# Performance work log

Hardware: AMD Instinct MI355X
Metric: run time of the kernel (lower is better)

The kernel has to match this reference:

```python
import jax, jax.numpy as jnp
import numpy as np

N = 40000          # nodes
E = 640000         # edges (avg in-degree ~16)
D_IN = 128         # in_dim == out_dim
E_DIM = 16         # edge feature dim
N_AGG = 6          # mean max min std dir1-av dir1-dx
N_SC = 3           # identity amplification attenuation
AVG_D_LOG = float(np.log(16.0))  # avg_d['log']
EPS = 1e-8
STD_EPS = 1e-5


def setup_inputs() -> dict:
    key = jax.random.key(0)
    ks = jax.random.split(key, 10)
    h = jax.random.normal(ks[0], (N, D_IN), jnp.float32)
    e = jax.random.normal(ks[1], (E, E_DIM), jnp.float32)
    eig = jax.random.normal(ks[2], (N, 2), jnp.float32)
    snorm_n = jax.random.uniform(ks[3], (N, 1), jnp.float32)
    src = jax.random.randint(ks[4], (E,), 0, N)
    dst = jax.random.randint(ks[5], (E,), 0, N)
    pre_in = 2 * D_IN + E_DIM
    W_pre = jax.random.normal(ks[6], (pre_in, D_IN), jnp.float32) / np.sqrt(pre_in)
    b_pre = jnp.zeros((D_IN,), jnp.float32)
    post_in = (N_AGG * N_SC + 1) * D_IN
    W_post = jax.random.normal(ks[7], (post_in, D_IN), jnp.float32) / np.sqrt(post_in)
    b_post = jnp.zeros((D_IN,), jnp.float32)
    return {"h": h, "e": e, "eig": eig, "snorm_n": snorm_n, "src": src,
            "dst": dst, "W_pre": W_pre, "b_pre": b_pre,
            "W_post": W_post, "b_post": b_post}


def reference(h, e, eig, snorm_n, src, dst, W_pre, b_pre, W_post, b_post):
    # --- pretrans on edges: MLP(cat(h_src, h_dst, ef)) -> [E, D_IN]
    z = jnp.concatenate([h[src], h[dst], e], axis=1)
    m = z @ W_pre + b_pre

    seg = lambda x: jax.ops.segment_sum(x, dst, num_segments=N)
    deg = seg(jnp.ones((E,), m.dtype))          # in-degree per node [N]
    has = deg > 0
    degc = jnp.maximum(deg, 1.0)

    # --- mailbox aggregators (edge-parallel segment reductions over dst)
    s1 = seg(m)
    mean = s1 / degc[:, None]
    var = seg(m * m) / degc[:, None] - mean * mean
    std = jnp.sqrt(jnp.maximum(var, 0.0) + STD_EPS)
    mx = jnp.where(has[:, None], jax.ops.segment_max(m, dst, num_segments=N), 0.0)
    mn = jnp.where(has[:, None], jax.ops.segment_min(m, dst, num_segments=N), 0.0)
    # eigenvector-directional aggregators (eig index 1), normalized per dst
    d = eig[src, 1] - eig[dst, 1]                              # [E]
    denom = seg(jnp.abs(d)) + EPS                              # [N]
    dir_av = seg(m * (jnp.abs(d) / denom[dst])[:, None])
    dir_dx = seg(m * (d / denom[dst])[:, None]) - h            # uses h_in

    agg = jnp.concatenate([mean, mx, mn, std, dir_av, dir_dx], axis=1)
    agg = jnp.where(has[:, None], agg, 0.0)  # DGL leaves zeros for isolated nodes

    # --- degree scalers: identity / amplification / attenuation
    logd = jnp.log(degc + 1.0)
    amp = agg * (logd / AVG_D_LOG)[:, None]
    att = agg * (AVG_D_LOG / logd)[:, None]
    hcat = jnp.concatenate([h, agg, amp, att], axis=1)  # [N, 19*D_IN]

    # --- posttrans MLP + graph norm + relu + residual (dropout p=0, no batchnorm)
    out = hcat @ W_post + b_post
    out = out * snorm_n
    out = jax.nn.relu(out)
    out = h + out
    return out
```

## Files before the change

kernel.cpp:

```cpp
#include <hip/hip_runtime.h>
#include <hip/hip_bf16.h>
#include <math.h>

typedef __attribute__((ext_vector_type(4))) float f32x4;
typedef __attribute__((ext_vector_type(2))) float f32x2;
typedef __attribute__((ext_vector_type(8))) short short8;
typedef unsigned short ushort_t;
typedef unsigned int uint_t;

__device__ __forceinline__ float b2f(unsigned short u) {
    unsigned int v = ((unsigned int)u) << 16;
    return __uint_as_float(v);
}
__device__ __forceinline__ unsigned short f2b(float f) {
    unsigned int x = __float_as_uint(f);
    unsigned int r = (x + 0x7fffu + ((x >> 16) & 1u)) >> 16;
    return (unsigned short)r;
}

__global__ void prep_kernel(const float* __restrict__ W_pre,
                            const float* __restrict__ W_post,
                            const float* __restrict__ h,
                            int* __restrict__ counts,
                            ushort_t* __restrict__ WbT,
                            ushort_t* __restrict__ WcT,
                            ushort_t* __restrict__ X, int Nn) {
    int i = blockIdx.x * 256 + threadIdx.x;
    int n0 = Nn + 1;
    if (i < n0) { counts[i] = 0; return; }
    i -= n0;
    if (i < 256 * 128) {
        int nn = i >> 7, k = i & 127;
        float v = (nn < 128) ? W_pre[k * 128 + nn] : W_pre[(128 + k) * 128 + (nn - 128)];
        WbT[i] = f2b(v);
        return;
    }
    i -= 256 * 128;
    if (i < 384 * 896) {
        int nn = i / 896, k = i % 896;
        float v;
        if (k < 128) {
            v = (nn < 128) ? W_post[k * 128 + nn] : 0.f;
        } else {
            int ka = k - 128;
            if (nn < 128)      v = W_post[(128 + ka) * 128 + nn];
            else if (nn < 256) v = W_post[(896 + ka) * 128 + (nn - 128)];
            else               v = W_post[(1664 + ka) * 128 + (nn - 256)];
        }
        WcT[i] = f2b(v);
        return;
    }
    i -= 384 * 896;
    if (i < Nn * 32) {
        int n = i >> 5, c4 = (i & 31) * 4;
        float4 hv = *(const float4*)&h[(size_t)n * 128 + c4];
        ushort4 o;
        o.x = f2b(hv.x); o.y = f2b(hv.y); o.z = f2b(hv.z); o.w = f2b(hv.w);
        *(ushort4*)&X[(size_t)n * 896 + c4] = o;
    }
}

__global__ void hist_kernel(const int* __restrict__ dst, int* __restrict__ counts, int E) {
    int i = blockIdx.x * 256 + threadIdx.x;
    if (i < E) atomicAdd(&counts[dst[i]], 1);
}

__global__ __launch_bounds__(256) void scanA_kernel(const int* __restrict__ counts,
                                                    int* __restrict__ localscan,
                                                    int* __restrict__ blocksum, int Nn) {
    __shared__ int part[256];
    int b = blockIdx.x, t = threadIdx.x;
    int idx = b * 1024 + t * 4;
    int4 v = (idx + 3 < Nn) ? *(const int4*)&counts[idx]
             : make_int4(idx < Nn ? counts[idx] : 0,
                         idx + 1 < Nn ? counts[idx + 1] : 0,
                         idx + 2 < Nn ? counts[idx + 2] : 0,
                         idx + 3 < Nn ? counts[idx + 3] : 0);
    int s1 = v.x, s2 = v.x + v.y, s3 = s2 + v.z, tot = s3 + v.w;
    part[t] = tot;
    __syncthreads();
    for (int off = 1; off < 256; off <<= 1) {
        int x = part[t];
        int u = (t >= off) ? part[t - off] : 0;
        __syncthreads();
        part[t] = x + u;
        __syncthreads();
    }
    int pre = (t > 0) ? part[t - 1] : 0;
    if (idx < Nn) {
        if (idx + 3 < Nn) {
            *(int4*)&localscan[idx] = make_int4(pre, pre + s1, pre + s2, pre + s3);
        } else {
            localscan[idx] = pre;
            if (idx + 1 < Nn) localscan[idx + 1] = pre + s1;
            if (idx + 2 < Nn) localscan[idx + 2] = pre + s2;
        }
    }
    if (t == 255) blocksum[b] = part[255];
}

__global__ __launch_bounds__(64) void scanB_kernel(int* __restrict__ blocksum, int nb) {
    __shared__ int sh[64];
    int t = threadIdx.x;
    int v = (t < nb) ? blocksum[t] : 0;
    sh[t] = v;
    __syncthreads();
    for (int off = 1; off < 64; off <<= 1) {
        int x = sh[t];
        int u = (t >= off) ? sh[t - off] : 0;
        __syncthreads();
        sh[t] = x + u;
        __syncthreads();
    }
    int pre = (t > 0) ? sh[t - 1] : 0;
    if (t < nb) blocksum[t] = pre;
    if (t == 63) blocksum[nb] = sh[63];
}

__global__ void scanC_kernel(int* __restrict__ localscan, const int* __restrict__ blocksum,
                             int* __restrict__ counts, int Nn, int nb) {
    int i = blockIdx.x * 256 + threadIdx.x;
    if (i < Nn) {
        int o = localscan[i] + blocksum[blockIdx.x >> 2];
        counts[i] = o;
        localscan[i] = o;
    }
    if (i == 0) counts[Nn] = blocksum[nb];
}

__global__ void scatter_kernel(const int* __restrict__ dst, const int* __restrict__ src,
                               const float* __restrict__ eig, int* __restrict__ cursors,
                               int4* __restrict__ esl, int E) {
    int i = blockIdx.x * 256 + threadIdx.x;
    if (i < E) {
        int v = dst[i];
        int p = atomicAdd(&cursors[v], 1);
        int s = src[i];
        esl[p] = make_int4(s, i, __float_as_int(eig[s * 2 + 1]), 0);
    }
}

template <int OUT_BF16>
__global__ __launch_bounds__(256) void gemm_bt(const ushort_t* __restrict__ A, int lda,
                                               const ushort_t* __restrict__ Bt, int ldb,
                                               void* __restrict__ Cv, int ldc,
                                               int M, int K, int NT) {
    __shared__ ushort_t ldsbuf[2 * 128 * 64];
    const int tid = threadIdx.x, wid = tid >> 6, lane = tid & 63;
    int nwg = gridDim.x;
    int orig = blockIdx.x;
    int q8 = nwg >> 3, r8 = nwg & 7;
    int xcd = orig & 7, local = orig >> 3;
    int wg = (xcd < r8 ? xcd * (q8 + 1) : r8 * (q8 + 1) + (xcd - r8) * q8) + local;
    const int m0 = (wg / NT) * 128, n0 = (wg % NT) * 128;
    f32x4 acc[4][4] = {};
    const int wrow = (wid >> 1) * 64, wcol = (wid & 1) * 64;

    for (int kt = 0; kt < K; kt += 64) {
#pragma unroll
        for (int rnd = 0; rnd < 4; ++rnd) {
            int libase = rnd * 256 + wid * 64;
            {
                int lc = libase + lane;
                int r = lc >> 3, cs = lc & 7;
                int c = cs ^ (r & 7);
                int row = m0 + r; row = row < M ? row : M - 1;
                const ushort_t* g = A + (size_t)row * lda + (kt + c * 8);
                __builtin_amdgcn_global_load_lds(
                    (const __attribute__((address_space(1))) unsigned int*)g,
                    (__attribute__((address_space(3))) unsigned int*)&ldsbuf[(size_t)libase * 8],
                    16, 0, 0);
            }
            {
                int lc = libase + lane;
                int r = lc >> 3, cs = lc & 7;
                int c = cs ^ (r & 7);
                const ushort_t* g = Bt + (size_t)(n0 + r) * ldb + (kt + c * 8);
                __builtin_amdgcn_global_load_lds(
                    (const __attribute__((address_space(1))) unsigned int*)g,
                    (__attribute__((address_space(3))) unsigned int*)&ldsbuf[8192 + (size_t)libase * 8],
                    16, 0, 0);
            }
        }
        __syncthreads();
#pragma unroll
        for (int kk = 0; kk < 2; ++kk) {
            short8 af[4], bfr[4];
#pragma unroll
            for (int f = 0; f < 4; ++f) {
                int r = wrow + f * 16 + (lane & 15);
                int c16 = kk * 4 + (lane >> 4);
                int ch = r * 8 + (c16 ^ (r & 7));
                af[f] = *(const short8*)&ldsbuf[ch * 8];
            }
#pragma unroll
            for (int f = 0; f < 4; ++f) {
                int r = wcol + f * 16 + (lane & 15);
                int c16 = kk * 4 + (lane >> 4);
                int ch = r * 8 + (c16 ^ (r & 7));
                bfr[f] = *(const short8*)&ldsbuf[8192 + ch * 8];
            }
#pragma unroll
            for (int i = 0; i < 4; ++i)
#pragma unroll
                for (int j = 0; j < 4; ++j)
                    acc[i][j] = __builtin_amdgcn_mfma_f32_16x16x32_bf16(af[i], bfr[j], acc[i][j], 0, 0, 0);
        }
        __syncthreads();
    }
#pragma unroll
    for (int i = 0; i < 4; ++i)
#pragma unroll
        for (int j = 0; j < 4; ++j)
#pragma unroll
            for (int q = 0; q < 4; ++q) {
                int row = m0 + wrow + i * 16 + (lane >> 4) * 4 + q;
                int col = n0 + wcol + j * 16 + (lane & 15);
                if (row < M) {
                    if (OUT_BF16) ((ushort_t*)Cv)[(size_t)row * ldc + col] = f2b(acc[i][j][q]);
                    else          ((float*)Cv)[(size_t)row * ldc + col] = acc[i][j][q];
                }
            }
}

#define RLI(v, l) __builtin_amdgcn_readlane((v), (l))
__global__ __launch_bounds__(256) void agg_coop(
    const ushort_t* __restrict__ PQ, ushort_t* __restrict__ X,
    const int4* __restrict__ esl, const int* __restrict__ offs,
    const float* __restrict__ eig, const float* __restrict__ h,
    const float* __restrict__ ef, const float* __restrict__ W_pre,
    const float* __restrict__ b_pre, float* __restrict__ scal, int Nn) {
    int tid = threadIdx.x;
    int wid = tid >> 6, lane = tid & 63;
    int n = blockIdx.x * 4 + wid;
    if (n >= Nn) return;
    int off0 = offs[n], off1 = offs[n + 1];
    int deg = off1 - off0;
    int d0 = lane * 2;

    f32x2 w3r[16];
#pragma unroll
    for (int j = 0; j < 16; ++j)
        w3r[j] = *(const f32x2*)&W_pre[(256 + j) * 128 + d0];

    uint_t qw = *(const uint_t*)&PQ[(size_t)n * 256 + 128 + d0];
    float2 bp = *(const float2*)&b_pre[d0];
    f32x2 qb;
    qb.x = b2f((ushort_t)(qw & 0xffff)) + bp.x;
    qb.y = b2f((ushort_t)(qw >> 16)) + bp.y;
    float eigd = eig[n * 2 + 1];

    f32x2 s = {0.f, 0.f}, ss = {0.f, 0.f}, av = {0.f, 0.f}, dv = {0.f, 0.f};
    f32x2 mx = {-1e30f, -1e30f}, mn = {1e30f, 1e30f};
    float den = 0.f;

    for (int q0 = off0; q0 < off1; q0 += 16) {
        int cnt = off1 - q0; if (cnt > 16) cnt = 16;
        int slot = q0 + (lane & 15);
        if (slot > off1 - 1) slot = off1 - 1;
        int4 rc = esl[slot];
        int eidL = __shfl(rc.y, lane >> 2);
        float4 efv = ((const float4*)ef)[(size_t)eidL * 4 + (lane & 3)];
        uint_t pw[16];
#pragma unroll
        for (int j = 0; j < 16; ++j) {
            if (j < cnt) {
                int sj = RLI(rc.x, j);
                pw[j] = *(const uint_t*)&PQ[(size_t)sj * 256 + d0];
            }
        }
#pragma unroll
        for (int j = 0; j < 16; ++j) {
            if (j < cnt) {
                f32x2 acc = qb;
#pragma unroll
                for (int b = 0; b < 4; ++b) {
                    float va = __uint_as_float((uint_t)RLI(__float_as_int(efv.x), 4 * j + b));
                    float vb = __uint_as_float((uint_t)RLI(__float_as_int(efv.y), 4 * j + b));
                    float vc = __uint_as_float((uint_t)RLI(__float_as_int(efv.z), 4 * j + b));
                    float vd = __uint_as_float((uint_t)RLI(__float_as_int(efv.w), 4 * j + b));
                    acc = va * w3r[4 * b + 0] + acc;
                    acc = vb * w3r[4 * b + 1] + acc;
                    acc = vc * w3r[4 * b + 2] + acc;
                    acc = vd * w3r[4 * b + 3] + acc;
                }
                f32x2 m;
                m.x = b2f((ushort_t)(pw[j] & 0xffff));
                m.y = b2f((ushort_t)(pw[j] >> 16));
                m = m + acc;
                float dd = __int_as_float(RLI(rc.z, j)) - eigd;
                float ad = fabsf(dd);
                s = s + m; ss = m * m + ss;
                mx = __builtin_elementwise_max(mx, m);
                mn = __builtin_elementwise_min(mn, m);
                av = ad * m + av; dv = dd * m + dv;
                den += ad;
            }
        }
    }

    size_t xb = (size_t)n * 896 + 128;
    float2 hv = *(const float2*)&h[(size_t)n * 128 + d0];
    float o[12];
    if (deg > 0) {
        float inv = 1.f / (float)deg;
        float mean0 = s.x * inv, mean1 = s.y * inv;
        float var0 = fmaxf(ss.x * inv - mean0 * mean0, 0.f);
        float var1 = fmaxf(ss.y * inv - mean1 * mean1, 0.f);
        float sd0 = sqrtf(var0 + 1e-5f), sd1 = sqrtf(var1 + 1e-5f);
        float idn = 1.f / (den + 1e-8f);
        o[0] = mean0; o[1] = mean1; o[2] = mx.x; o[3] = mx.y; o[4] = mn.x; o[5] = mn.y;
        o[6] = sd0; o[7] = sd1; o[8] = av.x * idn; o[9] = av.y * idn;
        o[10] = dv.x * idn - hv.x; o[11] = dv.y * idn - hv.y;
    } else {
#pragma unroll
        for (int k = 0; k < 12; ++k) o[k] = 0.f;
    }
#pragma unroll
    for (int a = 0; a < 6; ++a) {
        uint_t w = (uint_t)f2b(o[2 * a]) | ((uint_t)f2b(o[2 * a + 1]) << 16);
        *(uint_t*)&X[xb + a * 128 + d0] = w;
    }
    if (lane == 0) {
        float degc = deg > 0 ? (float)deg : 1.f;
        float logd = logf(degc + 1.f);
        scal[n * 2] = logd * (1.f / 2.772588722239781f);
        scal[n * 2 + 1] = 2.772588722239781f / logd;
    }
}

__global__ __launch_bounds__(256) void epilogue_kernel(
    const ushort_t* __restrict__ O3, const float* __restrict__ h,
    const float* __restrict__ snorm, const float* __restrict__ scal,
    const float* __restrict__ b_post, float* __restrict__ out, int Nn) {
    int g = blockIdx.x * 256 + threadIdx.x;
    if (g >= Nn * 32) return;
    int n = g >> 5, c4 = (g & 31) * 4;
    float a = scal[n * 2], b = scal[n * 2 + 1], sn = snorm[n];
    const ushort_t* base = O3 + (size_t)n * 384 + c4;
    ushort4 u1 = *(const ushort4*)base;
    ushort4 u2 = *(const ushort4*)(base + 128);
    ushort4 u3 = *(const ushort4*)(base + 256);
    float4 bp = *(const float4*)&b_post[c4];
    float4 hv = *(const float4*)&h[(size_t)n * 128 + c4];
    float4 r;
    r.x = fmaxf((b2f(u1.x) + a * b2f(u2.x) + b * b2f(u3.x) + bp.x) * sn, 0.f) + hv.x;
    r.y = fmaxf((b2f(u1.y) + a * b2f(u2.y) + b * b2f(u3.y) + bp.y) * sn, 0.f) + hv.y;
    r.z = fmaxf((b2f(u1.z) + a * b2f(u2.z) + b * b2f(u3.z) + bp.z) * sn, 0.f) + hv.z;
    r.w = fmaxf((b2f(u1.w) + a * b2f(u2.w) + b * b2f(u3.w) + bp.w) * sn, 0.f) + hv.w;
    *(float4*)&out[(size_t)n * 128 + c4] = r;
}

extern "C" void kernel_launch(void* const* d_in, const int* in_sizes, int n_in,
                              void* d_out, int out_size, void* d_ws, size_t ws_size,
                              hipStream_t stream) {
    const float* h      = (const float*)d_in[0];
    const float* ef     = (const float*)d_in[1];
    const float* eig    = (const float*)d_in[2];
    const float* snorm  = (const float*)d_in[3];
    const int*   src    = (const int*)d_in[4];
    const int*   dst    = (const int*)d_in[5];
    const float* W_pre  = (const float*)d_in[6];
    const float* b_pre  = (const float*)d_in[7];
    const float* W_post = (const float*)d_in[8];
    const float* b_post = (const float*)d_in[9];
    int Nn = in_sizes[0] / 128;
    int E  = in_sizes[4];
    float* out = (float*)d_out;

    char* ws = (char*)d_ws;
    size_t off = 0;
    auto alloc = [&](size_t bytes) {
        size_t o = off;
        off = (off + bytes + 255) & ~(size_t)255;
        return o;
    };
    size_t o_counts  = alloc(((size_t)Nn + 1) * 4);
    size_t o_cursors = alloc((size_t)Nn * 4);
    size_t o_bsum    = alloc(65 * 4);
    size_t o_esl     = alloc((size_t)E * 16);
    size_t o_PQ      = alloc((size_t)Nn * 256 * 2);
    size_t o_X       = alloc((size_t)Nn * 896 * 2);
    size_t o_O3      = alloc((size_t)Nn * 384 * 2);
    size_t o_scal    = alloc((size_t)Nn * 2 * 4);
    size_t o_wb      = alloc(256 * 128 * 2);
    size_t o_wc      = alloc(384 * 896 * 2);
    (void)ws_size;

    int*      counts  = (int*)(ws + o_counts);
    int*      cursors = (int*)(ws + o_cursors);
    int*      bsum    = (int*)(ws + o_bsum);
    int4*     esl     = (int4*)(ws + o_esl);
    ushort_t* PQ      = (ushort_t*)(ws + o_PQ);
    ushort_t* X       = (ushort_t*)(ws + o_X);
    ushort_t* O3      = (ushort_t*)(ws + o_O3);
    float*    scal    = (float*)(ws + o_scal);
    ushort_t* WbT     = (ushort_t*)(ws + o_wb);
    ushort_t* WcT     = (ushort_t*)(ws + o_wc);

    int prep_items = (Nn + 1) + 256 * 128 + 384 * 896 + Nn * 32;
    prep_kernel<<<(prep_items + 255) / 256, 256, 0, stream>>>(W_pre, W_post, h,
                                                              counts, WbT, WcT, X, Nn);
    hist_kernel<<<(E + 255) / 256, 256, 0, stream>>>(dst, counts, E);
    int nb = (Nn + 1023) / 1024;
    scanA_kernel<<<nb, 256, 0, stream>>>(counts, cursors, bsum, Nn);
    scanB_kernel<<<1, 64, 0, stream>>>(bsum, nb);
    scanC_kernel<<<(Nn + 255) / 256, 256, 0, stream>>>(cursors, bsum, counts, Nn, nb);
    scatter_kernel<<<(E + 255) / 256, 256, 0, stream>>>(dst, src, eig, cursors, esl, E);

    int mt = (Nn + 127) / 128;
    gemm_bt<1><<<mt * 2, 256, 0, stream>>>(X, 896, WbT, 128, (void*)PQ, 256, Nn, 128, 2);

    agg_coop<<<(Nn + 3) / 4, 256, 0, stream>>>(PQ, X, esl, counts, eig, h, ef,
                                               W_pre, b_pre, scal, Nn);

    gemm_bt<1><<<mt * 3, 256, 0, stream>>>(X, 896, WcT, 896, (void*)O3, 384, Nn, 896, 3);

    epilogue_kernel<<<(Nn * 32 + 255) / 256, 256, 0, stream>>>(O3, h, snorm, scal, b_post,
                                                               out, Nn);
}
```

Measured before the change: 226.8 us.

## Compute edge-feature projection with MFMA and permute feature layout in aggregation

The per-edge edge-feature projection (16-dim ef times W_pre rows 256..271) moves from scalar readlane FMAs to bf16 MFMA instructions inside the aggregation kernel. Each wave now handles 16 edges per MFMA, with lanes split into 4 edge groups and 16 column groups. Each lane owns 8 interleaved feature columns, so the PQ output and W_post rows are permuted to keep vectorized 16-byte loads and stores. This is meant to cut the heavy readlane/FMA cost of the edge MLP. In exchange it adds cross-lane shuffle reductions, bf16 rounding of the edge features, and permutation bookkeeping in the GEMM epilogue and weight prep.

```diff
diff --git a/kernel.cpp b/kernel.cpp
--- a/kernel.cpp
+++ b/kernel.cpp
@@ -5,6 +5,7 @@
 typedef __attribute__((ext_vector_type(4))) float f32x4;
 typedef __attribute__((ext_vector_type(2))) float f32x2;
 typedef __attribute__((ext_vector_type(8))) short short8;
+typedef __attribute__((ext_vector_type(4))) unsigned int uint4v;
 typedef unsigned short ushort_t;
 typedef unsigned int uint_t;
 
@@ -17,6 +18,8 @@
     unsigned int r = (x + 0x7fffu + ((x >> 16) & 1u)) >> 16;
     return (unsigned short)r;
 }
+
+__device__ __forceinline__ int permc(int d) { return ((d & 15) << 3) | (d >> 4); }
 
 __global__ void prep_kernel(const float* __restrict__ W_pre,
                             const float* __restrict__ W_post,
@@ -24,6 +27,7 @@
                             int* __restrict__ counts,
                             ushort_t* __restrict__ WbT,
                             ushort_t* __restrict__ WcT,
+                            ushort_t* __restrict__ W3P,
                             ushort_t* __restrict__ X, int Nn) {
     int i = blockIdx.x * 256 + threadIdx.x;
     int n0 = Nn + 1;
@@ -43,6 +47,9 @@
             v = (nn < 128) ? W_post[k * 128 + nn] : 0.f;
         } else {
             int ka = k - 128;
+            int pp = ka & 127;
+            int d = ((pp & 7) << 4) | (pp >> 3);
+            ka = (ka & ~127) | d;
             if (nn < 128)      v = W_post[(128 + ka) * 128 + nn];
             else if (nn < 256) v = W_post[(896 + ka) * 128 + (nn - 128)];
             else               v = W_post[(1664 + ka) * 128 + (nn - 256)];
@@ -51,6 +58,12 @@
         return;
     }
     i -= 384 * 896;
+    if (i < 128 * 16) {
+        int d = i >> 4, k = i & 15;
+        W3P[d * 16 + k] = f2b(W_pre[(256 + k) * 128 + d]);
+        return;
+    }
+    i -= 128 * 16;
     if (i < Nn * 32) {
         int n = i >> 5, c4 = (i & 31) * 4;
         float4 hv = *(const float4*)&h[(size_t)n * 128 + c4];
@@ -140,7 +153,7 @@
     }
 }
 
-template <int OUT_BF16>
+template <int OUT_BF16, int PERM>
 __global__ __launch_bounds__(256) void gemm_bt(const ushort_t* __restrict__ A, int lda,
                                                const ushort_t* __restrict__ Bt, int ldb,
                                                void* __restrict__ Cv, int ldc,
@@ -216,6 +229,7 @@
             for (int q = 0; q < 4; ++q) {
                 int row = m0 + wrow + i * 16 + (lane >> 4) * 4 + q;
                 int col = n0 + wcol + j * 16 + (lane & 15);
+                if (PERM) col = (col & ~127) | permc(col & 127);
                 if (row < M) {
                     if (OUT_BF16) ((ushort_t*)Cv)[(size_t)row * ldc + col] = f2b(acc[i][j][q]);
                     else          ((float*)Cv)[(size_t)row * ldc + col] = acc[i][j][q];
@@ -224,11 +238,11 @@
 }
 
 #define RLI(v, l) __builtin_amdgcn_readlane((v), (l))
-__global__ __launch_bounds__(256) void agg_coop(
+__global__ __launch_bounds__(256) void agg_mfma(
     const ushort_t* __restrict__ PQ, ushort_t* __restrict__ X,
     const int4* __restrict__ esl, const int* __restrict__ offs,
     const float* __restrict__ eig, const float* __restrict__ h,
-    const float* __restrict__ ef, const float* __restrict__ W_pre,
+    const float* __restrict__ ef, const ushort_t* __restrict__ W3P,
     const float* __restrict__ b_pre, float* __restrict__ scal, int Nn) {
     int tid = threadIdx.x;
     int wid = tid >> 6, lane = tid & 63;
@@ -236,93 +250,146 @@
     if (n >= Nn) return;
     int off0 = offs[n], off1 = offs[n + 1];
     int deg = off1 - off0;
-    int d0 = lane * 2;
-
-    f32x2 w3r[16];
-#pragma unroll
-    for (int j = 0; j < 16; ++j)
-        w3r[j] = *(const f32x2*)&W_pre[(256 + j) * 128 + d0];
-
-    uint_t qw = *(const uint_t*)&PQ[(size_t)n * 256 + 128 + d0];
-    float2 bp = *(const float2*)&b_pre[d0];
-    f32x2 qb;
-    qb.x = b2f((ushort_t)(qw & 0xffff)) + bp.x;
-    qb.y = b2f((ushort_t)(qw >> 16)) + bp.y;
+    int c = lane & 15, eg = lane >> 4;
+
+    const uint4v zu = {0u, 0u, 0u, 0u};
+    const short8 zf = __builtin_bit_cast(short8, zu);
+
+    short8 w3f[8];
+#pragma unroll
+    for (int b = 0; b < 8; ++b)
+        w3f[b] = (eg < 2) ? *(const short8*)&W3P[(b * 16 + c) * 16 + eg * 8] : zf;
+
+    float qb[8];
+    {
+        short8 qv = *(const short8*)&PQ[(size_t)n * 256 + 128 + c * 8];
+        uint4v qu = __builtin_bit_cast(uint4v, qv);
+#pragma unroll
+        for (int p = 0; p < 4; ++p) {
+            uint_t u = qu[p];
+            qb[2 * p]     = __uint_as_float(u << 16)          + b_pre[(2 * p) * 16 + c];
+            qb[2 * p + 1] = __uint_as_float(u & 0xffff0000u)  + b_pre[(2 * p + 1) * 16 + c];
+        }
+    }
     float eigd = eig[n * 2 + 1];
 
-    f32x2 s = {0.f, 0.f}, ss = {0.f, 0.f}, av = {0.f, 0.f}, dv = {0.f, 0.f};
-    f32x2 mx = {-1e30f, -1e30f}, mn = {1e30f, 1e30f};
+    float s[8] = {}, ssq[8] = {}, av[8] = {}, dv[8] = {};
+    float mx[8], mn[8];
+#pragma unroll
+    for (int b = 0; b < 8; ++b) { mx[b] = -1e30f; mn[b] = 1e30f; }
     float den = 0.f;
+    const f32x4 zeroc = {0.f, 0.f, 0.f, 0.f};
 
     for (int q0 = off0; q0 < off1; q0 += 16) {
-        int cnt = off1 - q0; if (cnt > 16) cnt = 16;
-        int slot = q0 + (lane & 15);
-        if (slot > off1 - 1) slot = off1 - 1;
+        int lim = off1 - 1;
+        int slot = q0 + c;
+        if (slot > lim) slot = lim;
         int4 rc = esl[slot];
-        int eidL = __shfl(rc.y, lane >> 2);
-        float4 efv = ((const float4*)ef)[(size_t)eidL * 4 + (lane & 3)];
-        uint_t pw[16];
-#pragma unroll
-        for (int j = 0; j < 16; ++j) {
-            if (j < cnt) {
-                int sj = RLI(rc.x, j);
-                pw[j] = *(const uint_t*)&PQ[(size_t)sj * 256 + d0];
-            }
-        }
-#pragma unroll
-        for (int j = 0; j < 16; ++j) {
-            if (j < cnt) {
-                f32x2 acc = qb;
-#pragma unroll
-                for (int b = 0; b < 4; ++b) {
-                    float va = __uint_as_float((uint_t)RLI(__float_as_int(efv.x), 4 * j + b));
-                    float vb = __uint_as_float((uint_t)RLI(__float_as_int(efv.y), 4 * j + b));
-                    float vc = __uint_as_float((uint_t)RLI(__float_as_int(efv.z), 4 * j + b));
-                    float vd = __uint_as_float((uint_t)RLI(__float_as_int(efv.w), 4 * j + b));
-                    acc = va * w3r[4 * b + 0] + acc;
-                    acc = vb * w3r[4 * b + 1] + acc;
-                    acc = vc * w3r[4 * b + 2] + acc;
-                    acc = vd * w3r[4 * b + 3] + acc;
-                }
-                f32x2 m;
-                m.x = b2f((ushort_t)(pw[j] & 0xffff));
-                m.y = b2f((ushort_t)(pw[j] >> 16));
-                m = m + acc;
-                float dd = __int_as_float(RLI(rc.z, j)) - eigd;
-                float ad = fabsf(dd);
-                s = s + m; ss = m * m + ss;
-                mx = __builtin_elementwise_max(mx, m);
-                mn = __builtin_elementwise_min(mn, m);
-                av = ad * m + av; dv = dd * m + dv;
-                den += ad;
-            }
-        }
-    }
-
+
+        short8 af = zf;
+        if (eg < 2) {
+            const float* ep = ef + (size_t)rc.y * 16 + eg * 8;
+            float4 e0 = *(const float4*)ep;
+            float4 e1 = *(const float4*)(ep + 4);
+            uint4v ua;
+            ua[0] = __builtin_amdgcn_perm(__float_as_uint(e0.y), __float_as_uint(e0.x), 0x07060302u);
+            ua[1] = __builtin_amdgcn_perm(__float_as_uint(e0.w), __float_as_uint(e0.z), 0x07060302u);
+            ua[2] = __builtin_amdgcn_perm(__float_as_uint(e1.y), __float_as_uint(e1.x), 0x07060302u);
+            ua[3] = __builtin_amdgcn_perm(__float_as_uint(e1.w), __float_as_uint(e1.z), 0x07060302u);
+            af = __builtin_bit_cast(short8, ua);
+        }
+
+        f32x4 acc[8];
+#pragma unroll
+        for (int b = 0; b < 8; ++b)
+            acc[b] = __builtin_amdgcn_mfma_f32_16x16x32_bf16(af, w3f[b], zeroc, 0, 0, 0);
+
+#pragma unroll
+        for (int q = 0; q < 4; ++q) {
+            int ei = eg * 4 + q;
+            int sj = __shfl(rc.x, ei);
+            float ddr = __int_as_float(__shfl(rc.z, ei)) - eigd;
+            bool valid = (q0 + ei) < off1;
+            float dd = valid ? ddr : 0.f;
+            float ad = fabsf(dd);
+            short8 pw = *(const short8*)&PQ[(size_t)sj * 256 + c * 8];
+            uint4v pu = __builtin_bit_cast(uint4v, pw);
+#pragma unroll
+            for (int p = 0; p < 4; ++p) {
+                uint_t u = pu[p];
+                float m0 = acc[2 * p][q]     + __uint_as_float(u << 16)         + qb[2 * p];
+                float m1 = acc[2 * p + 1][q] + __uint_as_float(u & 0xffff0000u) + qb[2 * p + 1];
+                mx[2 * p] = fmaxf(mx[2 * p], m0); mn[2 * p] = fminf(mn[2 * p], m0);
+                mx[2 * p + 1] = fmaxf(mx[2 * p + 1], m1); mn[2 * p + 1] = fminf(mn[2 * p + 1], m1);
+                float z0 = valid ? m0 : 0.f;
+                float z1 = valid ? m1 : 0.f;
+                s[2 * p] += z0; ssq[2 * p] = fmaf(z0, z0, ssq[2 * p]);
+                av[2 * p] = fmaf(z0, ad, av[2 * p]); dv[2 * p] = fmaf(z0, dd, dv[2 * p]);
+                s[2 * p + 1] += z1; ssq[2 * p + 1] = fmaf(z1, z1, ssq[2 * p + 1]);
+                av[2 * p + 1] = fmaf(z1, ad, av[2 * p + 1]); dv[2 * p + 1] = fmaf(z1, dd, dv[2 * p + 1]);
+            }
+            den += ad;
+        }
+    }
+
+#pragma unroll
+    for (int b = 0; b < 8; ++b) {
+        s[b] += __shfl_xor(s[b], 16);   s[b] += __shfl_xor(s[b], 32);
+        ssq[b] += __shfl_xor(ssq[b], 16); ssq[b] += __shfl_xor(ssq[b], 32);
+        av[b] += __shfl_xor(av[b], 16); av[b] += __shfl_xor(av[b], 32);
+        dv[b] += __shfl_xor(dv[b], 16); dv[b] += __shfl_xor(dv[b], 32);
+        mx[b] = fmaxf(mx[b], __shfl_xor(mx[b], 16)); mx[b] = fmaxf(mx[b], __shfl_xor(mx[b], 32));
+        mn[b] = fminf(mn[b], __shfl_xor(mn[b], 16)); mn[b] = fminf(mn[b], __shfl_xor(mn[b], 32));
+    }
+    den += __shfl_xor(den, 16); den += __shfl_xor(den, 32);
+
+    bool has = deg > 0;
+    float inv = has ? 1.f / (float)deg : 0.f;
+    float idn = has ? 1.f / (den + 1e-8f) : 0.f;
     size_t xb = (size_t)n * 896 + 128;
-    float2 hv = *(const float2*)&h[(size_t)n * 128 + d0];
-    float o[12];
-    if (deg > 0) {
-        float inv = 1.f / (float)deg;
-        float mean0 = s.x * inv, mean1 = s.y * inv;
-        float var0 = fmaxf(ss.x * inv - mean0 * mean0, 0.f);
-        float var1 = fmaxf(ss.y * inv - mean1 * mean1, 0.f);
-        float sd0 = sqrtf(var0 + 1e-5f), sd1 = sqrtf(var1 + 1e-5f);
-        float idn = 1.f / (den + 1e-8f);
-        o[0] = mean0; o[1] = mean1; o[2] = mx.x; o[3] = mx.y; o[4] = mn.x; o[5] = mn.y;
-        o[6] = sd0; o[7] = sd1; o[8] = av.x * idn; o[9] = av.y * idn;
-        o[10] = dv.x * idn - hv.x; o[11] = dv.y * idn - hv.y;
-    } else {
-#pragma unroll
-        for (int k = 0; k < 12; ++k) o[k] = 0.f;
-    }
-#pragma unroll
-    for (int a = 0; a < 6; ++a) {
-        uint_t w = (uint_t)f2b(o[2 * a]) | ((uint_t)f2b(o[2 * a + 1]) << 16);
-        *(uint_t*)&X[xb + a * 128 + d0] = w;
+
+    {
+        int a = eg;
+        ushort_t ob[8];
+#pragma unroll
+        for (int b = 0; b < 8; ++b) {
+            float val;
+            if (a == 0)      val = s[b] * inv;
+            else if (a == 1) val = mx[b];
+            else if (a == 2) val = mn[b];
+            else {
+                float mean = s[b] * inv;
+                float var = fmaxf(ssq[b] * inv - mean * mean, 0.f);
+                val = sqrtf(var + 1e-5f);
+            }
+            ob[b] = has ? f2b(val) : (ushort_t)0;
+        }
+        uint4v ou;
+        ou[0] = (uint_t)ob[0] | ((uint_t)ob[1] << 16);
+        ou[1] = (uint_t)ob[2] | ((uint_t)ob[3] << 16);
+        ou[2] = (uint_t)ob[4] | ((uint_t)ob[5] << 16);
+        ou[3] = (uint_t)ob[6] | ((uint_t)ob[7] << 16);
+        *(uint4v*)&X[xb + (size_t)a * 128 + c * 8] = ou;
+    }
+    if (eg < 2) {
+        int a = 4 + eg;
+        ushort_t ob[8];
+#pragma unroll
+        for (int b = 0; b < 8; ++b) {
+            float val;
+            if (a == 4) val = av[b] * idn;
+            else        val = dv[b] * idn - h[(size_t)n * 128 + b * 16 + c];
+            ob[b] = has ? f2b(val) : (ushort_t)0;
+        }
+        uint4v ou;
+        ou[0] = (uint_t)ob[0] | ((uint_t)ob[1] << 16);
+        ou[1] = (uint_t)ob[2] | ((uint_t)ob[3] << 16);
+        ou[2] = (uint_t)ob[4] | ((uint_t)ob[5] << 16);
+        ou[3] = (uint_t)ob[6] | ((uint_t)ob[7] << 16);
+        *(uint4v*)&X[xb + (size_t)a * 128 + c * 8] = ou;
     }
     if (lane == 0) {
-        float degc = deg > 0 ? (float)deg : 1.f;
+        float degc = has ? (float)deg : 1.f;
         float logd = logf(degc + 1.f);
         scal[n * 2] = logd * (1.f / 2.772588722239781f);
         scal[n * 2 + 1] = 2.772588722239781f / logd;
@@ -385,6 +452,7 @@
     size_t o_scal    = alloc((size_t)Nn * 2 * 4);
     size_t o_wb      = alloc(256 * 128 * 2);
     size_t o_wc      = alloc(384 * 896 * 2);
+    size_t o_w3p     = alloc(128 * 16 * 2);
     (void)ws_size;
 
     int*      counts  = (int*)(ws + o_counts);
@@ -397,10 +465,11 @@
     float*    scal    = (float*)(ws + o_scal);
     ushort_t* WbT     = (ushort_t*)(ws + o_wb);
     ushort_t* WcT     = (ushort_t*)(ws + o_wc);
-
-    int prep_items = (Nn + 1) + 256 * 128 + 384 * 896 + Nn * 32;
+    ushort_t* W3P     = (ushort_t*)(ws + o_w3p);
+
+    int prep_items = (Nn + 1) + 256 * 128 + 384 * 896 + 128 * 16 + Nn * 32;
     prep_kernel<<<(prep_items + 255) / 256, 256, 0, stream>>>(W_pre, W_post, h,
-                                                              counts, WbT, WcT, X, Nn);
+                                                              counts, WbT, WcT, W3P, X, Nn);
     hist_kernel<<<(E + 255) / 256, 256, 0, stream>>>(dst, counts, E);
     int nb = (Nn + 1023) / 1024;
     scanA_kernel<<<nb, 256, 0, stream>>>(counts, cursors, bsum, Nn);
@@ -409,12 +478,12 @@
     scatter_kernel<<<(E + 255) / 256, 256, 0, stream>>>(dst, src, eig, cursors, esl, E);
 
     int mt = (Nn + 127) / 128;
-    gemm_bt<1><<<mt * 2, 256, 0, stream>>>(X, 896, WbT, 128, (void*)PQ, 256, Nn, 128, 2);
-
-    agg_coop<<<(Nn + 3) / 4, 256, 0, stream>>>(PQ, X, esl, counts, eig, h, ef,
-                                               W_pre, b_pre, scal, Nn);
-
-    gemm_bt<1><<<mt * 3, 256, 0, stream>>>(X, 896, WcT, 896, (void*)O3, 384, Nn, 896, 3);
+    gemm_bt<1, 1><<<mt * 2, 256, 0, stream>>>(X, 896, WbT, 128, (void*)PQ, 256, Nn, 128, 2);
+
+    agg_mfma<<<(Nn + 3) / 4, 256, 0, stream>>>(PQ, X, esl, counts, eig, h, ef,
+                                               W3P, b_pre, scal, Nn);
+
+    gemm_bt<1, 0><<<mt * 3, 256, 0, stream>>>(X, 896, WcT, 896, (void*)O3, 384, Nn, 896, 3);
 
     epilogue_kernel<<<(Nn * 32 + 255) / 256, 256, 0, stream>>>(O3, h, snorm, scal, b_post,
                                                                out, Nn);
```

After: 295.8 us. 1.3x slower.
